# Performance work log

Hardware: AMD Instinct MI355X
Metric: run time of the kernel (lower is better)

The kernel has to match this reference:

```python
import jax, jax.numpy as jnp
import numpy as np

N_NODES = 100000
N_EDGES = 3200000
N_RELS = 8
F_IN = 64
F_OUT = 64


def setup_inputs() -> dict:
    key = jax.random.key(0)
    k1, k2, k3, k4, k5, k6 = jax.random.split(key, 6)
    X = jax.random.normal(k1, (N_NODES, F_IN), dtype=jnp.float32)
    W = jax.random.normal(k2, (N_RELS, F_IN, F_OUT), dtype=jnp.float32) * 0.1
    A = jax.random.uniform(k3, (N_EDGES,), dtype=jnp.float32)
    src = jax.random.randint(k4, (N_EDGES,), 0, N_NODES, dtype=jnp.int32)
    dst = jax.random.randint(k5, (N_EDGES,), 0, N_NODES, dtype=jnp.int32)
    etype = jax.random.randint(k6, (N_EDGES,), 0, N_RELS, dtype=jnp.int32)
    return {"X": X, "W": W, "A": A, "src": src, "dst": dst, "etype": etype}


def reference(X, W, A, src, dst, etype):
    # RGCN hetero forward: Y[i,fo] = sum_{r,j in N_r(i)} A[r,i,j] * (X[j] @ W[r])[fo]
    # Precompute per-relation transformed features: [R, N, F_out]
    XW = jnp.einsum('nf,rfo->rno', X, W)
    # Gather per-edge message and scale by edge weight: [E, F_out]
    msg = XW[etype, src] * A[:, None]
    # Scatter-add into destination nodes: [N, F_out]
    Y = jax.ops.segment_sum(msg, dst, num_segments=X.shape[0])
    return Y
```

## Files before the change

### kernel.cpp

```cpp
#include <hip/hip_runtime.h>
#include <hip/hip_fp16.h>

#define FDIM 64
#define P_BLK 1024
#define NSB_MAX 32
#define SB_BITS 12
#define SB_PAD 135168
#define CHUNK_CAP 3200
#define CHUNK2 4224
#define SPB 32
#define NB_MAX 800
#define BKT_NODES 128
#define SEG_PAD 4608
#define SEG_CAP 4608
#define OVF_CAP 64
#define CUR_STRIDE 16

typedef __attribute__((ext_vector_type(8))) short short8;
typedef __attribute__((ext_vector_type(4))) float float4_;

__device__ __forceinline__ unsigned short f2bf(float x) {
    unsigned u = __float_as_uint(x);
    return (unsigned short)((u + 0x7FFF + ((u >> 16) & 1)) >> 16);
}

__global__ __launch_bounds__(256) void xw_gemm_mfma(
    const float* __restrict__ X, const float* __restrict__ Wmat,
    __half* __restrict__ XWh, int N, int R)
{
    __shared__ unsigned short Wt[4 * 64 * 72];
    __shared__ unsigned short Ot[4][16 * 72];
    const int tid  = threadIdx.x;
    const int lane = tid & 63;
    const int wave = tid >> 6;
    const int quad = lane >> 4;
    const int l15  = lane & 15;
    const int rp   = blockIdx.y;
    const int blockBase = blockIdx.x * 256;

    short8 bfrag[4][2];
    bool tvalid[4];
#pragma unroll
    for (int t = 0; t < 4; ++t) {
        const int tb = blockBase + (wave * 4 + t) * 16;
        tvalid[t] = (tb < N);
        if (tvalid[t]) {
            const float* xp = X + (size_t)(tb + l15) * FDIM + quad * 8;
            const float4 x0 = *(const float4*)(xp);
            const float4 x1 = *(const float4*)(xp + 4);
            const float4 x2 = *(const float4*)(xp + 32);
            const float4 x3 = *(const float4*)(xp + 36);
            short8 b0, b1;
            b0[0]=f2bf(x0.x); b0[1]=f2bf(x0.y); b0[2]=f2bf(x0.z); b0[3]=f2bf(x0.w);
            b0[4]=f2bf(x1.x); b0[5]=f2bf(x1.y); b0[6]=f2bf(x1.z); b0[7]=f2bf(x1.w);
            b1[0]=f2bf(x2.x); b1[1]=f2bf(x2.y); b1[2]=f2bf(x2.z); b1[3]=f2bf(x2.w);
            b1[4]=f2bf(x3.x); b1[5]=f2bf(x3.y); b1[6]=f2bf(x3.z); b1[7]=f2bf(x3.w);
            bfrag[t][0] = b0; bfrag[t][1] = b1;
        } else {
            bfrag[t][0] = (short8)(0); bfrag[t][1] = (short8)(0);
        }
    }

#pragma unroll
    for (int it = 0; it < 16; ++it) {
        const int idx = it * 256 + tid;
        const int k  = idx & 63;
        const int f4 = (idx >> 6) & 15;
        const int r  = idx >> 10;
        const float4 w = *(const float4*)(Wmat + (((size_t)(rp * 4 + r) * FDIM + k) * FDIM + f4 * 4));
        const int base = (r * 64 + f4 * 4) * 72 + k;
        Wt[base + 0 * 72] = f2bf(w.x);
        Wt[base + 1 * 72] = f2bf(w.y);
        Wt[base + 2 * 72] = f2bf(w.z);
        Wt[base + 3 * 72] = f2bf(w.w);
    }
    __syncthreads();

#pragma unroll
    for (int t = 0; t < 4; ++t) {
        if (!tvalid[t]) continue;
        const int tb = blockBase + (wave * 4 + t) * 16;
#pragma unroll
        for (int r = 0; r < 4; ++r) {
#pragma unroll
            for (int ft = 0; ft < 4; ++ft) {
                const int f = ft * 16 + l15;
                const unsigned short* wp = &Wt[(r * 64 + f) * 72 + quad * 8];
                const short8 a0 = *(const short8*)(wp);
                const short8 a1 = *(const short8*)(wp + 32);
                float4_ acc = {0.f, 0.f, 0.f, 0.f};
                acc = __builtin_amdgcn_mfma_f32_16x16x32_bf16(a0, bfrag[t][0], acc, 0, 0, 0);
                acc = __builtin_amdgcn_mfma_f32_16x16x32_bf16(a1, bfrag[t][1], acc, 0, 0, 0);
                const __half2 h01 = __floats2half2_rn(acc[0], acc[1]);
                const __half2 h23 = __floats2half2_rn(acc[2], acc[3]);
                uint2 st;
                st.x = *(const unsigned*)&h01;
                st.y = *(const unsigned*)&h23;
                *(uint2*)&Ot[wave][l15 * 72 + ft * 16 + quad * 4] = st;
            }
            const int node = lane >> 2;
            const int c    = lane & 3;
            const uint4 w0 = *(const uint4*)&Ot[wave][node * 72 + c * 16];
            const uint4 w1 = *(const uint4*)&Ot[wave][node * 72 + c * 16 + 8];
            __half* orow = XWh + ((size_t)(rp * 4 + r) * N + (tb + node)) * FDIM;
            *(uint4*)(orow + c * 16)     = w0;
            *(uint4*)(orow + c * 16 + 8) = w1;
        }
    }
}

__global__ __launch_bounds__(1024) void init_cursors(
    int* __restrict__ gcur1, int* __restrict__ gcur2, int NSB, int B)
{
    const int t = (int)(blockIdx.x * 1024 + threadIdx.x);
    if (t < NSB) gcur1[t * CUR_STRIDE] = t * SB_PAD;
    if (t < B)   gcur2[t * CUR_STRIDE] = t * SEG_PAD;
}

__global__ __launch_bounds__(256) void scatter_coarse(
    const int* __restrict__ src, const int* __restrict__ dst,
    const int* __restrict__ etype, const float* __restrict__ A,
    int* __restrict__ gcur1, int2* __restrict__ packed1,
    int E, int N, int NSB, int chunk)
{
    __shared__ int lcnt[NSB_MAX];
    __shared__ int gb[NSB_MAX];
    __shared__ int2 recs[CHUNK_CAP];
    __shared__ unsigned char rbkt[CHUNK_CAP];
    const int p = blockIdx.x, tid = threadIdx.x;
    const int i0 = p * chunk, iend = min(i0 + chunk, E);

    if (tid < NSB_MAX) lcnt[tid] = 0;
    __syncthreads();
    for (int i = i0 + tid; i < iend; i += 256)
        atomicAdd(&lcnt[dst[i] >> SB_BITS], 1);
    __syncthreads();

    if (tid < 64) {
        const int c = (tid < NSB) ? lcnt[tid] : 0;
        int v = c;
#pragma unroll
        for (int o = 1; o < 64; o <<= 1) {
            const int u = __shfl_up(v, o, 64);
            if (tid >= o) v += u;
        }
        if (tid < NSB) gb[tid] = v - c;
    }
    __syncthreads();
    if (tid < NSB) {
        const int c = lcnt[tid];
        const int pfx = gb[tid];
        const int rbase = c ? atomicAdd(&gcur1[tid * CUR_STRIDE], c) : 0;
        gb[tid] = rbase - pfx;
        lcnt[tid] = pfx;
    }
    __syncthreads();

    for (int i = i0 + tid; i < iend; i += 256) {
        const int d = dst[i];
        const int sb = d >> SB_BITS;
        const int slot = atomicAdd(&lcnt[sb], 1);
        recs[slot] = make_int2((etype[i] * N + src[i]) | ((d & 127) << 20) | (((d >> 7) & 31) << 27),
                               __float_as_int(A[i]));
        rbkt[slot] = (unsigned char)sb;
    }
    __syncthreads();

    const int tot = iend - i0;
    for (int s = tid; s < tot; s += 256) {
        const int b = rbkt[s];
        const int gi = gb[b] + s;
        if (gi < (b + 1) * SB_PAD)
            packed1[gi] = recs[s];
    }
}

__global__ __launch_bounds__(256) void scatter_fine(
    const int2* __restrict__ packed1, const int* __restrict__ gcur1,
    int* __restrict__ gcur2, int2* __restrict__ packed2, int B)
{
    __shared__ int lcnt[32];
    __shared__ int gb[32];
    __shared__ int2 recs[CHUNK2];
    __shared__ unsigned char rbkt[CHUNK2];
    const int sb  = (int)blockIdx.x >> 5;
    const int cix = (int)blockIdx.x & 31;
    const int tid = threadIdx.x;
    const int sbBase = sb * SB_PAD;
    const int sbCnt = min(gcur1[sb * CUR_STRIDE] - sbBase, SB_PAD);
    const int i0 = cix * CHUNK2, iend = min(i0 + CHUNK2, sbCnt);
    if (i0 >= sbCnt) return;

    if (tid < 32) lcnt[tid] = 0;
    __syncthreads();
    for (int i = i0 + tid; i < iend; i += 256)
        atomicAdd(&lcnt[(packed1[sbBase + i].x >> 27) & 31], 1);
    __syncthreads();

    if (tid < 64) {
        const int c = (tid < 32) ? lcnt[tid] : 0;
        int v = c;
#pragma unroll
        for (int o = 1; o < 64; o <<= 1) {
            const int u = __shfl_up(v, o, 64);
            if (tid >= o) v += u;
        }
        if (tid < 32) gb[tid] = v - c;
    }
    __syncthreads();
    if (tid < 32) {
        const int bglob = sb * 32 + tid;
        const int c = lcnt[tid];
        const int pfx = gb[tid];
        const int rbase = (c && bglob < B) ? atomicAdd(&gcur2[bglob * CUR_STRIDE], c) : 0;
        gb[tid] = rbase - pfx;
        lcnt[tid] = pfx;
    }
    __syncthreads();

    for (int i = i0 + tid; i < iend; i += 256) {
        const int2 rec = packed1[sbBase + i];
        const int fb = (rec.x >> 27) & 31;
        const int slot = atomicAdd(&lcnt[fb], 1);
        recs[slot] = rec;
        rbkt[slot] = (unsigned char)fb;
    }
    __syncthreads();

    const int tot = iend - i0;
    for (int s = tid; s < tot; s += 256) {
        const int fb = rbkt[s];
        const int gi = gb[fb] + s;
        if (gi < (sb * 32 + fb + 1) * SEG_PAD)
            packed2[gi] = recs[s];
    }
}

__global__ __launch_bounds__(512) void agg_fused(
    const __half* __restrict__ XWh, const int2* __restrict__ packed,
    const int* __restrict__ gcur, float* __restrict__ Y, int N)
{
    __shared__ int2 recs[SEG_CAP];
    __shared__ int hist[BKT_NODES];
    __shared__ int pfx[BKT_NODES + 1];
    __shared__ int cur[BKT_NODES];
    __shared__ int2 ovf[OVF_CAP];
    __shared__ int ovfN;
    const int bkt = blockIdx.x, tid = threadIdx.x;
    const int segBase = bkt * SEG_PAD;
    const int cnt = min(gcur[bkt * CUR_STRIDE] - segBase, SEG_PAD);

    if (tid < BKT_NODES) hist[tid] = 0;
    if (tid == 0) ovfN = 0;
    __syncthreads();
    for (int i = tid; i < cnt; i += 512)
        atomicAdd(&hist[(packed[segBase + i].x >> 20) & 127], 1);
    __syncthreads();
    if (tid < 64) {
        int carry = 0;
#pragma unroll
        for (int t0 = 0; t0 < BKT_NODES; t0 += 64) {
            const int b = t0 + tid;
            const int c = hist[b];
            int v = c;
#pragma unroll
            for (int o = 1; o < 64; o <<= 1) {
                const int u = __shfl_up(v, o, 64);
                if (tid >= o) v += u;
            }
            pfx[b] = carry + v - c;
            cur[b] = carry + v - c;
            carry += __shfl(v, 63, 64);
            if (tid == 0 && t0 + 64 == BKT_NODES) pfx[BKT_NODES] = carry;
        }
    }
    __syncthreads();
    for (int i = tid; i < cnt; i += 512) {
        const int2 rec = packed[segBase + i];
        const int dl = (rec.x >> 20) & 127;
        const int pos = atomicAdd(&cur[dl], 1);
        if (pos < SEG_CAP) recs[pos] = rec;
        else { const int o = atomicAdd(&ovfN, 1); if (o < OVF_CAP) ovf[o] = rec; }
    }
    __syncthreads();

    const int lane = tid & 63;
    const int w    = tid >> 6;
    const int el   = lane >> 4;
    const int fl4  = lane & 15;
    const __half2* __restrict__ XW2 = (const __half2*)XWh;
    const unsigned foff = (unsigned)(fl4 << 1);

    for (int j = 0; j < 16; ++j) {
        const int nl = w * 16 + j;
        const int gnode = bkt * BKT_NODES + nl;
        if (gnode >= N) break;
        const int beg = min(pfx[nl], SEG_CAP);
        const int end = min(pfx[nl + 1], SEG_CAP);
        float4_ acc = {0.f, 0.f, 0.f, 0.f};
        for (int b2 = beg; b2 < end; b2 += 64) {
            const int idx = b2 + lane;
            const int2 ka = (idx < end) ? recs[idx] : make_int2(0, 0);
            const int nb = min(64, end - b2);
            const int nsteps = (((nb + 3) >> 2) + 7) & ~7;
            for (int s = 0; s < nsteps; s += 8) {
                int k[8], bv[8];
#pragma unroll
                for (int u = 0; u < 8; ++u) {
                    const int jj = ((s + u) << 2) + el;
                    k[u]  = __shfl(ka.x, jj, 64);
                    bv[u] = __shfl(ka.y, jj, 64);
                }
                uint2 v[8];
#pragma unroll
                for (int u = 0; u < 8; ++u)
                    v[u] = *(const uint2*)(XW2 + ((((unsigned)k[u]) & 0xFFFFFu) << 5) + foff);
#pragma unroll
                for (int u = 0; u < 8; ++u) {
                    const float a = __int_as_float(bv[u]);
                    const float2 f0 = __half22float2(*(const __half2*)&v[u].x);
                    const float2 f1 = __half22float2(*(const __half2*)&v[u].y);
                    acc[0] += a * f0.x; acc[1] += a * f0.y;
                    acc[2] += a * f1.x; acc[3] += a * f1.y;
                }
            }
        }
#pragma unroll
        for (int m = 16; m <= 32; m <<= 1) {
            acc[0] += __shfl_xor(acc[0], m, 64);
            acc[1] += __shfl_xor(acc[1], m, 64);
            acc[2] += __shfl_xor(acc[2], m, 64);
            acc[3] += __shfl_xor(acc[3], m, 64);
        }
        if (lane < 16)
            *(float4_*)(Y + (size_t)gnode * FDIM + (fl4 << 2)) = acc;
    }
    __syncthreads();

    const int no = min(ovfN, OVF_CAP);
    for (int o = tid; o < no; o += 512) {
        const int2 rec = ovf[o];
        const int node = bkt * BKT_NODES + ((rec.x >> 20) & 127);
        if (node < N) {
            const float a = __int_as_float(rec.y);
            const __half* row = XWh + (size_t)(rec.x & 0xFFFFF) * FDIM;
            for (int f = 0; f < FDIM; ++f)
                atomicAdd(&Y[(size_t)node * FDIM + f], a * __half2float(row[f]));
        }
    }
}

extern "C" void kernel_launch(void* const* d_in, const int* in_sizes, int n_in,
                              void* d_out, int out_size, void* d_ws, size_t ws_size,
                              hipStream_t stream)
{
    const float* X     = (const float*)d_in[0];
    const float* Wmat  = (const float*)d_in[1];
    const float* A     = (const float*)d_in[2];
    const int*   src   = (const int*)d_in[3];
    const int*   dst   = (const int*)d_in[4];
    const int*   etype = (const int*)d_in[5];
    float* Y = (float*)d_out;

    const int N = in_sizes[0] / FDIM;
    const int R = in_sizes[1] / (FDIM * FDIM);
    const int E = in_sizes[2];
    (void)n_in; (void)out_size; (void)ws_size;

    const int B   = (N + BKT_NODES - 1) / BKT_NODES;
    const int NSB = (N + (1 << SB_BITS) - 1) >> SB_BITS;
    const int chunk = (E + P_BLK - 1) / P_BLK;

    char* ws = (char*)d_ws;
    size_t off = 0;
    auto take = [&](size_t bytes) { char* p = ws + off; off = (off + bytes + 255) & ~(size_t)255; return p; };
    __half* XWh     = (__half*)take((size_t)R * N * FDIM * sizeof(__half));
    int2*   packed1 = (int2*)  take((size_t)NSB * SB_PAD * sizeof(int2));
    int2*   packed2 = (int2*)  take((size_t)B * SEG_PAD * sizeof(int2));
    int*    gcur1   = (int*)   take((size_t)NSB * CUR_STRIDE * sizeof(int));
    int*    gcur2   = (int*)   take((size_t)B * CUR_STRIDE * sizeof(int));

    init_cursors<<<1, 1024, 0, stream>>>(gcur1, gcur2, NSB, B);
    xw_gemm_mfma<<<dim3((N + 255) / 256, (R + 3) / 4), 256, 0, stream>>>(X, Wmat, XWh, N, R);
    scatter_coarse<<<P_BLK, 256, 0, stream>>>(src, dst, etype, A, gcur1, packed1, E, N, NSB, chunk);
    scatter_fine<<<NSB * SPB, 256, 0, stream>>>(packed1, gcur1, gcur2, packed2, B);
    agg_fused<<<B, 512, 0, stream>>>(XWh, packed2, gcur2, Y, N);
}
```

Baseline: 291.9 us.

## Fuse XW GEMM and coarse edge scatter into one interleaved launch

```diff
diff --git a/kernel.cpp b/kernel.cpp
--- a/kernel.cpp
+++ b/kernel.cpp
@@ -15,6 +15,7 @@
 #define SEG_CAP 4608
 #define OVF_CAP 64
 #define CUR_STRIDE 16
+#define FUSED_LDS 46080
 
 typedef __attribute__((ext_vector_type(8))) short short8;
 typedef __attribute__((ext_vector_type(4))) float float4_;
@@ -24,91 +25,6 @@
     return (unsigned short)((u + 0x7FFF + ((u >> 16) & 1)) >> 16);
 }
 
-__global__ __launch_bounds__(256) void xw_gemm_mfma(
-    const float* __restrict__ X, const float* __restrict__ Wmat,
-    __half* __restrict__ XWh, int N, int R)
-{
-    __shared__ unsigned short Wt[4 * 64 * 72];
-    __shared__ unsigned short Ot[4][16 * 72];
-    const int tid  = threadIdx.x;
-    const int lane = tid & 63;
-    const int wave = tid >> 6;
-    const int quad = lane >> 4;
-    const int l15  = lane & 15;
-    const int rp   = blockIdx.y;
-    const int blockBase = blockIdx.x * 256;
-
-    short8 bfrag[4][2];
-    bool tvalid[4];
-#pragma unroll
-    for (int t = 0; t < 4; ++t) {
-        const int tb = blockBase + (wave * 4 + t) * 16;
-        tvalid[t] = (tb < N);
-        if (tvalid[t]) {
-            const float* xp = X + (size_t)(tb + l15) * FDIM + quad * 8;
-            const float4 x0 = *(const float4*)(xp);
-            const float4 x1 = *(const float4*)(xp + 4);
-            const float4 x2 = *(const float4*)(xp + 32);
-            const float4 x3 = *(const float4*)(xp + 36);
-            short8 b0, b1;
-            b0[0]=f2bf(x0.x); b0[1]=f2bf(x0.y); b0[2]=f2bf(x0.z); b0[3]=f2bf(x0.w);
-            b0[4]=f2bf(x1.x); b0[5]=f2bf(x1.y); b0[6]=f2bf(x1.z); b0[7]=f2bf(x1.w);
-            b1[0]=f2bf(x2.x); b1[1]=f2bf(x2.y); b1[2]=f2bf(x2.z); b1[3]=f2bf(x2.w);
-            b1[4]=f2bf(x3.x); b1[5]=f2bf(x3.y); b1[6]=f2bf(x3.z); b1[7]=f2bf(x3.w);
-            bfrag[t][0] = b0; bfrag[t][1] = b1;
-        } else {
-            bfrag[t][0] = (short8)(0); bfrag[t][1] = (short8)(0);
-        }
-    }
-
-#pragma unroll
-    for (int it = 0; it < 16; ++it) {
-        const int idx = it * 256 + tid;
-        const int k  = idx & 63;
-        const int f4 = (idx >> 6) & 15;
-        const int r  = idx >> 10;
-        const float4 w = *(const float4*)(Wmat + (((size_t)(rp * 4 + r) * FDIM + k) * FDIM + f4 * 4));
-        const int base = (r * 64 + f4 * 4) * 72 + k;
-        Wt[base + 0 * 72] = f2bf(w.x);
-        Wt[base + 1 * 72] = f2bf(w.y);
-        Wt[base + 2 * 72] = f2bf(w.z);
-        Wt[base + 3 * 72] = f2bf(w.w);
-    }
-    __syncthreads();
-
-#pragma unroll
-    for (int t = 0; t < 4; ++t) {
-        if (!tvalid[t]) continue;
-        const int tb = blockBase + (wave * 4 + t) * 16;
-#pragma unroll
-        for (int r = 0; r < 4; ++r) {
-#pragma unroll
-            for (int ft = 0; ft < 4; ++ft) {
-                const int f = ft * 16 + l15;
-                const unsigned short* wp = &Wt[(r * 64 + f) * 72 + quad * 8];
-                const short8 a0 = *(const short8*)(wp);
-                const short8 a1 = *(const short8*)(wp + 32);
-                float4_ acc = {0.f, 0.f, 0.f, 0.f};
-                acc = __builtin_amdgcn_mfma_f32_16x16x32_bf16(a0, bfrag[t][0], acc, 0, 0, 0);
-                acc = __builtin_amdgcn_mfma_f32_16x16x32_bf16(a1, bfrag[t][1], acc, 0, 0, 0);
-                const __half2 h01 = __floats2half2_rn(acc[0], acc[1]);
-                const __half2 h23 = __floats2half2_rn(acc[2], acc[3]);
-                uint2 st;
-                st.x = *(const unsigned*)&h01;
-                st.y = *(const unsigned*)&h23;
-                *(uint2*)&Ot[wave][l15 * 72 + ft * 16 + quad * 4] = st;
-            }
-            const int node = lane >> 2;
-            const int c    = lane & 3;
-            const uint4 w0 = *(const uint4*)&Ot[wave][node * 72 + c * 16];
-            const uint4 w1 = *(const uint4*)&Ot[wave][node * 72 + c * 16 + 8];
-            __half* orow = XWh + ((size_t)(rp * 4 + r) * N + (tb + node)) * FDIM;
-            *(uint4*)(orow + c * 16)     = w0;
-            *(uint4*)(orow + c * 16 + 8) = w1;
-        }
-    }
-}
-
 __global__ __launch_bounds__(1024) void init_cursors(
     int* __restrict__ gcur1, int* __restrict__ gcur2, int NSB, int B)
 {
@@ -117,61 +33,152 @@
     if (t < B)   gcur2[t * CUR_STRIDE] = t * SEG_PAD;
 }
 
-__global__ __launch_bounds__(256) void scatter_coarse(
+__global__ __launch_bounds__(256) void gemm_coarse_fused(
+    const float* __restrict__ X, const float* __restrict__ Wmat,
+    __half* __restrict__ XWh,
     const int* __restrict__ src, const int* __restrict__ dst,
     const int* __restrict__ etype, const float* __restrict__ A,
     int* __restrict__ gcur1, int2* __restrict__ packed1,
-    int E, int N, int NSB, int chunk)
-{
-    __shared__ int lcnt[NSB_MAX];
-    __shared__ int gb[NSB_MAX];
-    __shared__ int2 recs[CHUNK_CAP];
-    __shared__ unsigned char rbkt[CHUNK_CAP];
-    const int p = blockIdx.x, tid = threadIdx.x;
-    const int i0 = p * chunk, iend = min(i0 + chunk, E);
-
-    if (tid < NSB_MAX) lcnt[tid] = 0;
-    __syncthreads();
-    for (int i = i0 + tid; i < iend; i += 256)
-        atomicAdd(&lcnt[dst[i] >> SB_BITS], 1);
-    __syncthreads();
-
-    if (tid < 64) {
-        const int c = (tid < NSB) ? lcnt[tid] : 0;
-        int v = c;
-#pragma unroll
-        for (int o = 1; o < 64; o <<= 1) {
-            const int u = __shfl_up(v, o, 64);
-            if (tid >= o) v += u;
-        }
-        if (tid < NSB) gb[tid] = v - c;
-    }
-    __syncthreads();
-    if (tid < NSB) {
-        const int c = lcnt[tid];
-        const int pfx = gb[tid];
-        const int rbase = c ? atomicAdd(&gcur1[tid * CUR_STRIDE], c) : 0;
-        gb[tid] = rbase - pfx;
-        lcnt[tid] = pfx;
-    }
-    __syncthreads();
-
-    for (int i = i0 + tid; i < iend; i += 256) {
-        const int d = dst[i];
-        const int sb = d >> SB_BITS;
-        const int slot = atomicAdd(&lcnt[sb], 1);
-        recs[slot] = make_int2((etype[i] * N + src[i]) | ((d & 127) << 20) | (((d >> 7) & 31) << 27),
-                               __float_as_int(A[i]));
-        rbkt[slot] = (unsigned char)sb;
-    }
-    __syncthreads();
-
-    const int tot = iend - i0;
-    for (int s = tid; s < tot; s += 256) {
-        const int b = rbkt[s];
-        const int gi = gb[b] + s;
-        if (gi < (b + 1) * SB_PAD)
-            packed1[gi] = recs[s];
+    int E, int N, int R, int NSB, int chunk, int gemmBlocks, int totalBlocks)
+{
+    extern __shared__ char smem[];
+    const int bid = (int)blockIdx.x;
+    const int tid = threadIdx.x;
+    const int gcount = (int)(((long)bid * gemmBlocks) / totalBlocks);
+    const int gnext  = (int)(((long)(bid + 1) * gemmBlocks) / totalBlocks);
+
+    if (gnext > gcount) {
+        unsigned short* Wt = (unsigned short*)smem;
+        unsigned short* Ot = Wt + 4 * 64 * 72;
+        const int gb_id = gcount;
+        const int rp    = gb_id & 1;
+        const int blockBase = (gb_id >> 1) * 256;
+        const int lane = tid & 63;
+        const int wave = tid >> 6;
+        const int quad = lane >> 4;
+        const int l15  = lane & 15;
+        unsigned short* Otw = Ot + wave * 16 * 72;
+
+        short8 bfrag[4][2];
+        bool tvalid[4];
+#pragma unroll
+        for (int t = 0; t < 4; ++t) {
+            const int tb = blockBase + (wave * 4 + t) * 16;
+            tvalid[t] = (tb < N);
+            if (tvalid[t]) {
+                const float* xp = X + (size_t)(tb + l15) * FDIM + quad * 8;
+                const float4 x0 = *(const float4*)(xp);
+                const float4 x1 = *(const float4*)(xp + 4);
+                const float4 x2 = *(const float4*)(xp + 32);
+                const float4 x3 = *(const float4*)(xp + 36);
+                short8 b0, b1;
+                b0[0]=f2bf(x0.x); b0[1]=f2bf(x0.y); b0[2]=f2bf(x0.z); b0[3]=f2bf(x0.w);
+                b0[4]=f2bf(x1.x); b0[5]=f2bf(x1.y); b0[6]=f2bf(x1.z); b0[7]=f2bf(x1.w);
+                b1[0]=f2bf(x2.x); b1[1]=f2bf(x2.y); b1[2]=f2bf(x2.z); b1[3]=f2bf(x2.w);
+                b1[4]=f2bf(x3.x); b1[5]=f2bf(x3.y); b1[6]=f2bf(x3.z); b1[7]=f2bf(x3.w);
+                bfrag[t][0] = b0; bfrag[t][1] = b1;
+            } else {
+                bfrag[t][0] = (short8)(0); bfrag[t][1] = (short8)(0);
+            }
+        }
+
+#pragma unroll
+        for (int it = 0; it < 16; ++it) {
+            const int idx = it * 256 + tid;
+            const int k  = idx & 63;
+            const int f4 = (idx >> 6) & 15;
+            const int r  = idx >> 10;
+            const float4 w = *(const float4*)(Wmat + (((size_t)(rp * 4 + r) * FDIM + k) * FDIM + f4 * 4));
+            const int base = (r * 64 + f4 * 4) * 72 + k;
+            Wt[base + 0 * 72] = f2bf(w.x);
+            Wt[base + 1 * 72] = f2bf(w.y);
+            Wt[base + 2 * 72] = f2bf(w.z);
+            Wt[base + 3 * 72] = f2bf(w.w);
+        }
+        __syncthreads();
+
+#pragma unroll
+        for (int t = 0; t < 4; ++t) {
+            if (!tvalid[t]) continue;
+            const int tb = blockBase + (wave * 4 + t) * 16;
+#pragma unroll
+            for (int r = 0; r < 4; ++r) {
+#pragma unroll
+                for (int ft = 0; ft < 4; ++ft) {
+                    const int f = ft * 16 + l15;
+                    const unsigned short* wp = &Wt[(r * 64 + f) * 72 + quad * 8];
+                    const short8 a0 = *(const short8*)(wp);
+                    const short8 a1 = *(const short8*)(wp + 32);
+                    float4_ acc = {0.f, 0.f, 0.f, 0.f};
+                    acc = __builtin_amdgcn_mfma_f32_16x16x32_bf16(a0, bfrag[t][0], acc, 0, 0, 0);
+                    acc = __builtin_amdgcn_mfma_f32_16x16x32_bf16(a1, bfrag[t][1], acc, 0, 0, 0);
+                    const __half2 h01 = __floats2half2_rn(acc[0], acc[1]);
+                    const __half2 h23 = __floats2half2_rn(acc[2], acc[3]);
+                    uint2 st;
+                    st.x = *(const unsigned*)&h01;
+                    st.y = *(const unsigned*)&h23;
+                    *(uint2*)&Otw[l15 * 72 + ft * 16 + quad * 4] = st;
+                }
+                const int node = lane >> 2;
+                const int c    = lane & 3;
+                const uint4 w0 = *(const uint4*)&Otw[node * 72 + c * 16];
+                const uint4 w1 = *(const uint4*)&Otw[node * 72 + c * 16 + 8];
+                __half* orow = XWh + ((size_t)(rp * 4 + r) * N + (tb + node)) * FDIM;
+                *(uint4*)(orow + c * 16)     = w0;
+                *(uint4*)(orow + c * 16 + 8) = w1;
+            }
+        }
+    } else {
+        int* lcnt = (int*)smem;
+        int* gb   = lcnt + NSB_MAX;
+        int2* recs = (int2*)(smem + 256);
+        unsigned char* rbkt = (unsigned char*)(recs + CHUNK_CAP);
+        const int p = bid - gcount;
+        const int i0 = p * chunk, iend = min(i0 + chunk, E);
+
+        if (tid < NSB_MAX) lcnt[tid] = 0;
+        __syncthreads();
+        for (int i = i0 + tid; i < iend; i += 256)
+            atomicAdd(&lcnt[dst[i] >> SB_BITS], 1);
+        __syncthreads();
+
+        if (tid < 64) {
+            const int c = (tid < NSB) ? lcnt[tid] : 0;
+            int v = c;
+#pragma unroll
+            for (int o = 1; o < 64; o <<= 1) {
+                const int u = __shfl_up(v, o, 64);
+                if (tid >= o) v += u;
+            }
+            if (tid < NSB) gb[tid] = v - c;
+        }
+        __syncthreads();
+        if (tid < NSB) {
+            const int c = lcnt[tid];
+            const int pfx = gb[tid];
+            const int rbase = c ? atomicAdd(&gcur1[tid * CUR_STRIDE], c) : 0;
+            gb[tid] = rbase - pfx;
+            lcnt[tid] = pfx;
+        }
+        __syncthreads();
+
+        for (int i = i0 + tid; i < iend; i += 256) {
+            const int d = dst[i];
+            const int sb = d >> SB_BITS;
+            const int slot = atomicAdd(&lcnt[sb], 1);
+            recs[slot] = make_int2((etype[i] * N + src[i]) | ((d & 127) << 20) | (((d >> 7) & 31) << 27),
+                                   __float_as_int(A[i]));
+            rbkt[slot] = (unsigned char)sb;
+        }
+        __syncthreads();
+
+        const int tot = iend - i0;
+        for (int s = tid; s < tot; s += 256) {
+            const int b = rbkt[s];
+            const int gi = gb[b] + s;
+            if (gi < (b + 1) * SB_PAD)
+                packed1[gi] = recs[s];
+        }
     }
 }
 
@@ -370,6 +377,8 @@
     const int B   = (N + BKT_NODES - 1) / BKT_NODES;
     const int NSB = (N + (1 << SB_BITS) - 1) >> SB_BITS;
     const int chunk = (E + P_BLK - 1) / P_BLK;
+    const int gemmBlocks  = ((N + 255) / 256) * 2;
+    const int totalBlocks = gemmBlocks + P_BLK;
 
     char* ws = (char*)d_ws;
     size_t off = 0;
@@ -381,8 +390,9 @@
     int*    gcur2   = (int*)   take((size_t)B * CUR_STRIDE * sizeof(int));
 
     init_cursors<<<1, 1024, 0, stream>>>(gcur1, gcur2, NSB, B);
-    xw_gemm_mfma<<<dim3((N + 255) / 256, (R + 3) / 4), 256, 0, stream>>>(X, Wmat, XWh, N, R);
-    scatter_coarse<<<P_BLK, 256, 0, stream>>>(src, dst, etype, A, gcur1, packed1, E, N, NSB, chunk);
+    gemm_coarse_fused<<<totalBlocks, 256, FUSED_LDS, stream>>>(
+        X, Wmat, XWh, src, dst, etype, A, gcur1, packed1,
+        E, N, R, NSB, chunk, gemmBlocks, totalBlocks);
     scatter_fine<<<NSB * SPB, 256, 0, stream>>>(packed1, gcur1, gcur2, packed2, B);
     agg_fused<<<B, 512, 0, stream>>>(XWh, packed2, gcur2, Y, N);
 }
```

Result: no change. 287.4 us (-1.6%).
